# Optimization experiments

Measured on AMD Instinct MI355X. Metric: run time of the kernel, lower is better.

## Reference

```python
import jax, jax.numpy as jnp
import numpy as np

N_NODES = 65536
IN_DIM = 256
HIDDEN = 256
NUM_GRAPHS = 128   # B = batch.max()+1; fixed by construction in setup_inputs
MAX_LEN = 1024     # >= max per-graph length (avg 512, binomial tail << 1024)


def _uniform(key, shape, scale):
    return jax.random.uniform(key, shape, jnp.float32, -scale, scale)


def setup_inputs() -> dict:
    key = jax.random.key(0)
    ks = jax.random.split(key, 12)
    x = jax.random.normal(ks[0], (N_NODES, IN_DIM), jnp.float32)
    batch = jnp.sort(jax.random.randint(ks[1], (N_NODES,), 0, NUM_GRAPHS)).astype(jnp.int64)
    s = 1.0 / np.sqrt(HIDDEN)  # torch nn.GRU init: U(-1/sqrt(H), 1/sqrt(H))
    # gate order follows torch: (r, z, n) stacked along first axis -> 3H rows
    params = {
        'W_ih0': _uniform(ks[2], (3 * HIDDEN, IN_DIM), s),
        'W_hh0': _uniform(ks[3], (3 * HIDDEN, HIDDEN), s),
        'b_ih0': _uniform(ks[4], (3 * HIDDEN,), s),
        'b_hh0': _uniform(ks[5], (3 * HIDDEN,), s),
        'W_ih1': _uniform(ks[6], (3 * HIDDEN, HIDDEN), s),
        'W_hh1': _uniform(ks[7], (3 * HIDDEN, HIDDEN), s),
        'b_ih1': _uniform(ks[8], (3 * HIDDEN,), s),
        'b_hh1': _uniform(ks[9], (3 * HIDDEN,), s),
    }
    return {'x': x, 'batch': batch, **params}


def _gru_layer(xs, W_ih, W_hh, b_ih, b_hh):
    # xs: [B, L, D] -> [B, L, H]; torch GRU cell math, gate order (r, z, n)
    B = xs.shape[0]
    H = W_hh.shape[1]
    gx = jnp.einsum('bld,gd->blg', xs, W_ih) + b_ih  # precompute input gates, one big GEMM

    def step(h, gx_t):
        gh = h @ W_hh.T + b_hh
        xr, xz, xn = jnp.split(gx_t, 3, axis=-1)
        hr, hz, hn = jnp.split(gh, 3, axis=-1)
        r = jax.nn.sigmoid(xr + hr)
        z = jax.nn.sigmoid(xz + hz)
        n = jnp.tanh(xn + r * hn)
        h_new = (1.0 - z) * n + z * h
        return h_new, h_new

    h0 = jnp.zeros((B, H), xs.dtype)
    _, hs = jax.lax.scan(step, h0, jnp.swapaxes(gx, 0, 1))  # [L, B, H]
    return jnp.swapaxes(hs, 0, 1)


def reference(x, batch, W_ih0, W_hh0, b_ih0, b_hh0, W_ih1, W_hh1, b_ih1, b_hh1):
    # Ragged per-graph sequences -> padded [B, MAX_LEN, D]. Padding is at the
    # end of each row; GRU is causal so valid positions match the per-graph
    # loop in the original module exactly, and the masked mean ignores padding.
    N, D = x.shape
    b32 = batch.astype(jnp.int32)
    counts = jax.ops.segment_sum(jnp.ones((N,), jnp.float32), b32, num_segments=NUM_GRAPHS)
    starts = jnp.cumsum(counts) - counts              # exclusive prefix sum
    pos = jnp.arange(N, dtype=jnp.float32) - starts[b32]
    pos = pos.astype(jnp.int32)                       # position within graph

    xp = jnp.zeros((NUM_GRAPHS, MAX_LEN, D), x.dtype).at[b32, pos].set(x)
    mask = jnp.zeros((NUM_GRAPHS, MAX_LEN), x.dtype).at[b32, pos].set(1.0)

    h = _gru_layer(xp, W_ih0, W_hh0, b_ih0, b_hh0)
    h = _gru_layer(h, W_ih1, W_hh1, b_ih1, b_hh1)

    denom = jnp.maximum(counts, 1.0)[:, None]
    out = jnp.sum(h * mask[:, :, None], axis=1) / denom  # mean over valid steps
    return out  # dropout is identity at eval
```

## Files before the change

### kernel.cpp

```cpp
#include <hip/hip_runtime.h>
#include <hip/hip_bf16.h>

typedef _Float16 half2_t __attribute__((ext_vector_type(2)));
typedef _Float16 f16x8   __attribute__((ext_vector_type(8)));
typedef float    f32x4   __attribute__((ext_vector_type(4)));
typedef unsigned short u16;
typedef unsigned int   u32;

#define N_NODES 65536
#define IN_DIM  256
#define HIDDEN  256
#define G3      768
#define NGRAPH  128

__device__ __forceinline__ float sigf(float x)    { return 1.f / (1.f + __expf(-x)); }
__device__ __forceinline__ float tanhfast(float x){ return 2.f / (1.f + __expf(-2.f * x)) - 1.f; }

__device__ __forceinline__ void mfma_a(f32x4& acc, const f16x8& a, const f16x8& b) {
    asm("v_mfma_f32_16x16x32_f16 %0, %1, %2, %0" : "+v"(acc) : "a"(a), "v"(b));
}
__device__ __forceinline__ void mfma_v(f32x4& acc, const f16x8& a, const f16x8& b) {
    asm("v_mfma_f32_16x16x32_f16 %0, %1, %2, %0" : "+v"(acc) : "v"(a), "v"(b));
}
__device__ __forceinline__ void mfma_az(f32x4& acc, const f16x8& a, const f16x8& b, const f32x4& z) {
    asm("v_mfma_f32_16x16x32_f16 %0, %1, %2, %3" : "=&v"(acc) : "a"(a), "v"(b), "v"(z));
}
__device__ __forceinline__ void mfma_vz(f32x4& acc, const f16x8& a, const f16x8& b, const f32x4& z) {
    asm("v_mfma_f32_16x16x32_f16 %0, %1, %2, %3" : "=&v"(acc) : "v"(a), "v"(b), "v"(z));
}

__device__ __forceinline__ void wg_barrier_lds() {
    asm volatile("s_waitcnt lgkmcnt(0)" ::: "memory");
    __builtin_amdgcn_s_barrier();
}

__global__ void k_starts(const int* __restrict__ batch, int* __restrict__ starts, int n, int ngraph) {
    int g = blockIdx.x * blockDim.x + threadIdx.x;
    if (g > ngraph) return;
    int stride = (batch[n - 1] == 0) ? 2 : 1;
    if (g == ngraph) { starts[g] = n; return; }
    int lo = 0, hi = n;
    while (lo < hi) { int mid = (lo + hi) >> 1; if (batch[(size_t)mid * stride] < g) lo = mid + 1; else hi = mid; }
    starts[g] = lo;
}

__global__ void k_cvt8(const float* __restrict__ s, u16* __restrict__ d, int n) {
    int t = blockIdx.x * 256 + threadIdx.x;
    int i = t * 8;
    if (i >= n) return;
    float4 a = ((const float4*)(s + i))[0];
    float4 b = ((const float4*)(s + i))[1];
    f16x8 o;
    o[0] = (_Float16)a.x; o[1] = (_Float16)a.y; o[2] = (_Float16)a.z; o[3] = (_Float16)a.w;
    o[4] = (_Float16)b.x; o[5] = (_Float16)b.y; o[6] = (_Float16)b.z; o[7] = (_Float16)b.w;
    *(f16x8*)(d + i) = o;
}

__global__ void k_bias(const float* __restrict__ bih, const float* __restrict__ bhh, float* __restrict__ o) {
    int i = blockIdx.x * 256 + threadIdx.x;
    if (i < G3) o[i] = bih[i] + (i < 512 ? bhh[i] : 0.f);
}

__global__ void k_swz(const float* __restrict__ W, uint4* __restrict__ out) {
    int t = blockIdx.x * 256 + threadIdx.x;
    if (t >= 24576) return;
    int l = t & 63, c = t >> 6;
    int kt = c & 7, t6 = (c >> 3) % 12, wv = c / 96;
    int rg = t6 >> 2, sub = t6 & 3;
    int row = rg * 256 + wv * 64 + sub * 16 + (l & 15);
    int col = kt * 32 + (l >> 4) * 8;
    const float* s = W + row * 256 + col;
    f16x8 o;
#pragma unroll
    for (int q = 0; q < 8; q++) o[q] = (_Float16)s[q];
    out[t] = __builtin_bit_cast(uint4, o);
}

template <typename AT>
__global__ __launch_bounds__(256) void k_gemm(
    const AT* __restrict__ A, const u16* __restrict__ Bm,
    const float* __restrict__ bias, u16* __restrict__ C,
    int M, int N, int K)
{
    __shared__ u16 As[128 * 40];
    __shared__ u16 Bs[128 * 40];
    const int m0 = blockIdx.y * 128, n0 = blockIdx.x * 128;
    const int t = threadIdx.x;
    const int wave = t >> 6, lane = t & 63;
    const int wm = wave & 1, wn = wave >> 1;
    const int lr = lane & 15, lq = lane >> 4;
    f32x4 acc[4][4] = {};
    const int sr = t >> 1, sp = t & 1;
    const AT*  gA = A  + (size_t)(m0 + sr) * K + sp * 16;
    const u16* gB = Bm + (size_t)(n0 + sr) * K + sp * 16;
    u16* sA = As + sr * 40 + sp * 16;
    u16* sB = Bs + sr * 40 + sp * 16;
    for (int kt = 0; kt < K; kt += 32) {
        uint4 av0, av1;
        if constexpr (sizeof(AT) == 4) {
            float4 a0 = ((const float4*)gA)[0], a1 = ((const float4*)gA)[1];
            float4 a2 = ((const float4*)gA)[2], a3 = ((const float4*)gA)[3];
            f16x8 lo, hi;
            lo[0]=(_Float16)a0.x; lo[1]=(_Float16)a0.y; lo[2]=(_Float16)a0.z; lo[3]=(_Float16)a0.w;
            lo[4]=(_Float16)a1.x; lo[5]=(_Float16)a1.y; lo[6]=(_Float16)a1.z; lo[7]=(_Float16)a1.w;
            hi[0]=(_Float16)a2.x; hi[1]=(_Float16)a2.y; hi[2]=(_Float16)a2.z; hi[3]=(_Float16)a2.w;
            hi[4]=(_Float16)a3.x; hi[5]=(_Float16)a3.y; hi[6]=(_Float16)a3.z; hi[7]=(_Float16)a3.w;
            av0 = __builtin_bit_cast(uint4, lo);
            av1 = __builtin_bit_cast(uint4, hi);
        } else {
            av0 = ((const uint4*)gA)[0];
            av1 = ((const uint4*)gA)[1];
        }
        uint4 b0 = ((const uint4*)gB)[0], b1 = ((const uint4*)gB)[1];
        gA += 32; gB += 32;
        __syncthreads();
        ((uint4*)sA)[0] = av0; ((uint4*)sA)[1] = av1;
        ((uint4*)sB)[0] = b0;  ((uint4*)sB)[1] = b1;
        __syncthreads();
        f16x8 af[4], bf[4];
#pragma unroll
        for (int i = 0; i < 4; i++)
            af[i] = *(const f16x8*)(As + (wm * 64 + i * 16 + lr) * 40 + lq * 8);
#pragma unroll
        for (int j = 0; j < 4; j++)
            bf[j] = *(const f16x8*)(Bs + (wn * 64 + j * 16 + lr) * 40 + lq * 8);
#pragma unroll
        for (int i = 0; i < 4; i++)
#pragma unroll
            for (int j = 0; j < 4; j++)
                acc[i][j] = __builtin_amdgcn_mfma_f32_16x16x32_f16(af[i], bf[j], acc[i][j], 0, 0, 0);
    }
#pragma unroll
    for (int i = 0; i < 4; i++) {
        int row = m0 + wm * 64 + i * 16 + lq * 4;
#pragma unroll
        for (int j = 0; j < 4; j++) {
            int col = n0 + wn * 64 + j * 16 + lr;
            float bv = bias[col];
#pragma unroll
            for (int rr = 0; rr < 4; rr++) {
                _Float16 v = (_Float16)(acc[i][j][rr] + bv);
                C[(size_t)(row + rr) * N + col] = __builtin_bit_cast(u16, v);
            }
        }
    }
}

__global__ __attribute__((amdgpu_flat_work_group_size(256, 256), amdgpu_waves_per_eu(1, 1)))
void k_rec(
    const u16* __restrict__ gx,
    const uint4* __restrict__ wsw,
    const float* __restrict__ bhh,
    const int*   __restrict__ starts,
    u16* __restrict__ hout,
    float* __restrict__ out)
{
    __shared__ float gates[G3];
    __shared__ uint4 hbuf[2][HIDDEN / 8];
    const int g = blockIdx.x;
    const int tid = threadIdx.x;
    const int l = tid & 63, wv = tid >> 6;
    const int start = starts[g];
    const int len = starts[g + 1] - start;
    if (tid < HIDDEN / 8) hbuf[0][tid] = make_uint4(0, 0, 0, 0);
    f16x8 wa[60], wb[36];
    {
        const uint4* p = wsw + (size_t)wv * 96 * 64 + l;
#pragma unroll
        for (int f = 0; f < 60; f++) {
            f16x8 v = __builtin_bit_cast(f16x8, p[f * 64]);
            asm volatile("" : "+a"(v));
            wa[f] = v;
        }
#pragma unroll
        for (int f = 0; f < 36; f++) {
            f16x8 v = __builtin_bit_cast(f16x8, p[(60 + f) * 64]);
            asm volatile("" : "+v"(v));
            wb[f] = v;
        }
    }
    const _Float16* gxr = (const _Float16*)gx + (size_t)start * G3 + tid;
    u16* hb = hout ? (hout + (size_t)start * HIDDEN + tid) : (u16*)nullptr;
    float hp = 0.f, hs = 0.f;
    const float bn = bhh[512 + tid];
    const f32x4 zf = {0.f, 0.f, 0.f, 0.f};
    float c_r = 0.f, c_z = 0.f, c_n = 0.f;
    float n_r = 0.f, n_z = 0.f, n_n = 0.f;
    if (len > 0) {
        c_r = (float)gxr[0]; c_z = (float)gxr[256]; c_n = (float)gxr[512];
        int t1 = len > 1 ? 1 : 0;
        const _Float16* p = gxr + (u32)t1 * G3;
        n_r = (float)p[0]; n_z = (float)p[256]; n_n = (float)p[512];
    }
    __syncthreads();
    for (int t = 0; t < len; ++t) {
        int t2 = t + 2 < len ? t + 2 : len - 1;
        const _Float16* pp = gxr + (u32)t2 * G3;
        float l_r = (float)pp[0], l_z = (float)pp[256], l_n = (float)pp[512];
        f32x4 acc[12];
#pragma unroll
        for (int kt = 0; kt < 8; kt++) {
            f16x8 b = __builtin_bit_cast(f16x8, hbuf[t & 1][kt * 4 + (l >> 4)]);
#pragma unroll
            for (int t6 = 0; t6 < 12; t6++) {
                const int f = t6 * 8 + kt;
                if (kt == 0) {
                    if (f < 60) mfma_az(acc[t6], wa[f], b, zf);
                    else        mfma_vz(acc[t6], wb[f - 60], b, zf);
                } else {
                    if (f < 60) mfma_a(acc[t6], wa[f], b);
                    else        mfma_v(acc[t6], wb[f - 60], b);
                }
            }
        }
        asm volatile("s_nop 7\n\ts_nop 7"
                     : "+v"(acc[0]), "+v"(acc[1]), "+v"(acc[2]), "+v"(acc[3]),
                       "+v"(acc[4]), "+v"(acc[5]), "+v"(acc[6]), "+v"(acc[7]),
                       "+v"(acc[8]), "+v"(acc[9]), "+v"(acc[10]), "+v"(acc[11]));
        if ((l & 15) == 0) {
#pragma unroll
            for (int t6 = 0; t6 < 12; t6++) {
                int ro = (t6 >> 2) * 256 + wv * 64 + (t6 & 3) * 16 + (l >> 4) * 4;
                *(f32x4*)&gates[ro] = acc[t6];
            }
        }
        {
            float r = sigf(c_r + gates[tid]);
            float z = sigf(c_z + gates[256 + tid]);
            float n = tanhfast(c_n + r * (gates[512 + tid] + bn));
            float hnew = (1.f - z) * n + z * hp;
            hp = hnew; hs += hnew;
            _Float16 ph = (_Float16)hnew;
            u16 pk = __builtin_bit_cast(u16, ph);
            ((u16*)hbuf[(t + 1) & 1])[tid] = pk;
            if (hb) hb[(u32)t * HIDDEN] = pk;
            c_r = n_r; c_z = n_z; c_n = n_n;
            n_r = l_r; n_z = l_z; n_n = l_n;
        }
        wg_barrier_lds();
    }
    if (out) {
        float inv = 1.f / (float)(len > 0 ? len : 1);
        out[g * HIDDEN + tid] = hs * inv;
    }
}

extern "C" void kernel_launch(void* const* d_in, const int* in_sizes, int n_in,
                              void* d_out, int out_size, void* d_ws, size_t ws_size,
                              hipStream_t stream)
{
    const float* x     = (const float*)d_in[0];
    const int*   batch = (const int*)d_in[1];
    const float* Wih0  = (const float*)d_in[2];
    const float* Whh0  = (const float*)d_in[3];
    const float* bih0  = (const float*)d_in[4];
    const float* bhh0  = (const float*)d_in[5];
    const float* Wih1  = (const float*)d_in[6];
    const float* Whh1  = (const float*)d_in[7];
    const float* bih1  = (const float*)d_in[8];
    const float* bhh1  = (const float*)d_in[9];
    float* out = (float*)d_out;

    char* ws = (char*)d_ws;
    size_t o = 0;
    int*   starts = (int*)  (ws + o); o += 4096;
    float* bias0  = (float*)(ws + o); o += 4096;
    float* bias1  = (float*)(ws + o); o += 4096;
    u16*   wi0    = (u16*)  (ws + o); o += (size_t)G3 * IN_DIM * 2;
    u16*   wi1    = (u16*)  (ws + o); o += (size_t)G3 * HIDDEN * 2;
    uint4* wsw0   = (uint4*)(ws + o); o += (size_t)G3 * HIDDEN * 2;
    uint4* wsw1   = (uint4*)(ws + o); o += (size_t)G3 * HIDDEN * 2;
    u16*   h0     = (u16*)  (ws + o); o += (size_t)N_NODES * HIDDEN * 2;
    u16*   gxbuf  = (u16*)  (ws + o); o += (size_t)N_NODES * G3 * 2;

    k_starts<<<1, 256, 0, stream>>>(batch, starts, N_NODES, NGRAPH);
    k_bias<<<3, 256, 0, stream>>>(bih0, bhh0, bias0);
    k_bias<<<3, 256, 0, stream>>>(bih1, bhh1, bias1);
    k_cvt8<<<96, 256, 0, stream>>>(Wih0, wi0, G3 * IN_DIM);
    k_cvt8<<<96, 256, 0, stream>>>(Wih1, wi1, G3 * HIDDEN);
    k_swz<<<96, 256, 0, stream>>>(Whh0, wsw0);
    k_swz<<<96, 256, 0, stream>>>(Whh1, wsw1);

    k_gemm<float><<<dim3(G3 / 128, N_NODES / 128), 256, 0, stream>>>(x, wi0, bias0, gxbuf, N_NODES, G3, IN_DIM);
    k_rec<<<NGRAPH, 256, 0, stream>>>(gxbuf, wsw0, bhh0, starts, h0, (float*)nullptr);
    k_gemm<_Float16><<<dim3(G3 / 128, N_NODES / 128), 256, 0, stream>>>((const _Float16*)h0, wi1, bias1, gxbuf, N_NODES, G3, HIDDEN);
    k_rec<<<NGRAPH, 256, 0, stream>>>(gxbuf, wsw1, bhh1, starts, (u16*)nullptr, out);
}
```

Before: 1.782 ms.

## Interleave two graphs per recurrent block to overlap MFMA with gate math

Each recurrent workgroup now handles two graphs, A and B, and alternates between them. The MFMA matvec for one graph is issued while the elementwise gate update of the other runs, which hides MFMA latency and the barrier stall behind independent work. The grid is halved, so only 64 blocks run on the many CUs and each block's time is the longer of its two graphs' lengths. Sched barriers are added around the workgroup barrier, and the AGPR/VGPR weight split moves from 60/36 to 64/32.

Result: slower. 3.755 ms (+110.7%).

```diff
diff --git a/kernel.cpp b/kernel.cpp
--- a/kernel.cpp
+++ b/kernel.cpp
@@ -30,8 +30,11 @@
 }
 
 __device__ __forceinline__ void wg_barrier_lds() {
+    __builtin_amdgcn_sched_barrier(0);
     asm volatile("s_waitcnt lgkmcnt(0)" ::: "memory");
+    __builtin_amdgcn_sched_barrier(0);
     __builtin_amdgcn_s_barrier();
+    __builtin_amdgcn_sched_barrier(0);
 }
 
 __global__ void k_starts(const int* __restrict__ batch, int* __restrict__ starts, int n, int ngraph) {
@@ -155,93 +158,106 @@
     u16* __restrict__ hout,
     float* __restrict__ out)
 {
-    __shared__ float gates[G3];
-    __shared__ uint4 hbuf[2][HIDDEN / 8];
-    const int g = blockIdx.x;
+    __shared__ float gatesA[G3], gatesB[G3];
+    __shared__ uint4 hbA[2][HIDDEN / 8], hbB[2][HIDDEN / 8];
     const int tid = threadIdx.x;
     const int l = tid & 63, wv = tid >> 6;
-    const int start = starts[g];
-    const int len = starts[g + 1] - start;
-    if (tid < HIDDEN / 8) hbuf[0][tid] = make_uint4(0, 0, 0, 0);
-    f16x8 wa[60], wb[36];
+    const int gA = blockIdx.x, gB = blockIdx.x + NGRAPH / 2;
+    const int startA = starts[gA], lenA = starts[gA + 1] - startA;
+    const int startB = starts[gB], lenB = starts[gB + 1] - startB;
+    if (tid < HIDDEN / 8) { hbA[0][tid] = make_uint4(0,0,0,0); hbB[0][tid] = make_uint4(0,0,0,0); }
+    f16x8 wa[64], wb[32];
     {
         const uint4* p = wsw + (size_t)wv * 96 * 64 + l;
 #pragma unroll
-        for (int f = 0; f < 60; f++) {
+        for (int f = 0; f < 64; f++) {
             f16x8 v = __builtin_bit_cast(f16x8, p[f * 64]);
             asm volatile("" : "+a"(v));
             wa[f] = v;
         }
 #pragma unroll
-        for (int f = 0; f < 36; f++) {
-            f16x8 v = __builtin_bit_cast(f16x8, p[(60 + f) * 64]);
+        for (int f = 0; f < 32; f++) {
+            f16x8 v = __builtin_bit_cast(f16x8, p[(64 + f) * 64]);
             asm volatile("" : "+v"(v));
             wb[f] = v;
         }
     }
-    const _Float16* gxr = (const _Float16*)gx + (size_t)start * G3 + tid;
-    u16* hb = hout ? (hout + (size_t)start * HIDDEN + tid) : (u16*)nullptr;
-    float hp = 0.f, hs = 0.f;
+    const _Float16* gxrA = (const _Float16*)gx + (size_t)startA * G3 + tid;
+    const _Float16* gxrB = (const _Float16*)gx + (size_t)startB * G3 + tid;
+    u16* hoA = hout ? (hout + (size_t)startA * HIDDEN + tid) : (u16*)nullptr;
+    u16* hoB = hout ? (hout + (size_t)startB * HIDDEN + tid) : (u16*)nullptr;
     const float bn = bhh[512 + tid];
     const f32x4 zf = {0.f, 0.f, 0.f, 0.f};
-    float c_r = 0.f, c_z = 0.f, c_n = 0.f;
-    float n_r = 0.f, n_z = 0.f, n_n = 0.f;
-    if (len > 0) {
-        c_r = (float)gxr[0]; c_z = (float)gxr[256]; c_n = (float)gxr[512];
-        int t1 = len > 1 ? 1 : 0;
-        const _Float16* p = gxr + (u32)t1 * G3;
-        n_r = (float)p[0]; n_z = (float)p[256]; n_n = (float)p[512];
-    }
+    float hpA = 0.f, hsA = 0.f, hpB = 0.f, hsB = 0.f;
+    float aR = 0.f, aZ = 0.f, aN = 0.f, bR = 0.f, bZ = 0.f, bN = 0.f;
+    if (lenA > 0) { aR = (float)gxrA[0]; aZ = (float)gxrA[256]; aN = (float)gxrA[512]; }
+    if (lenB > 0) { bR = (float)gxrB[0]; bZ = (float)gxrB[256]; bN = (float)gxrB[512]; }
+    f32x4 accA[12], accB[12];
+
+#define MFMA_STEP(ACC, HBBUF)                                                   \
+    do {                                                                        \
+        _Pragma("unroll")                                                       \
+        for (int kt = 0; kt < 8; kt++) {                                        \
+            f16x8 b = __builtin_bit_cast(f16x8, (HBBUF)[kt * 4 + (l >> 4)]);    \
+            _Pragma("unroll")                                                   \
+            for (int t6 = 0; t6 < 12; t6++) {                                   \
+                const int f = t6 * 8 + kt;                                      \
+                if (kt == 0) { if (f < 64) mfma_az(ACC[t6], wa[f], b, zf);      \
+                               else        mfma_vz(ACC[t6], wb[f - 64], b, zf);}\
+                else         { if (f < 64) mfma_a(ACC[t6], wa[f], b);           \
+                               else        mfma_v(ACC[t6], wb[f - 64], b); }    \
+            }                                                                   \
+        }                                                                       \
+    } while (0)
+
+#define NOP_FENCE(ACC)                                                          \
+    asm volatile("s_nop 7\n\ts_nop 7"                                           \
+                 : "+v"(ACC[0]), "+v"(ACC[1]), "+v"(ACC[2]), "+v"(ACC[3]),      \
+                   "+v"(ACC[4]), "+v"(ACC[5]), "+v"(ACC[6]), "+v"(ACC[7]),      \
+                   "+v"(ACC[8]), "+v"(ACC[9]), "+v"(ACC[10]), "+v"(ACC[11]))
+
+#define FIN_STEP(ACC, GATES, HBARR, CR, CZ, CN, HP, HS, HOP, GXR, LEN, I)       \
+    do {                                                                        \
+        int inx_ = (I) + 1 < (LEN) ? (I) + 1 : (LEN) - 1;                       \
+        const _Float16* pp_ = (GXR) + (u32)inx_ * G3;                           \
+        float pR_ = (float)pp_[0], pZ_ = (float)pp_[256], pN_ = (float)pp_[512];\
+        NOP_FENCE(ACC);                                                         \
+        if ((l & 15) == 0) {                                                    \
+            _Pragma("unroll")                                                   \
+            for (int t6 = 0; t6 < 12; t6++) {                                   \
+                int ro = (t6 >> 2) * 256 + wv * 64 + (t6 & 3) * 16 + (l >> 4) * 4;\
+                *(f32x4*)&(GATES)[ro] = ACC[t6];                                \
+            }                                                                   \
+        }                                                                       \
+        float r_ = sigf((CR) + (GATES)[tid]);                                   \
+        float z_ = sigf((CZ) + (GATES)[256 + tid]);                             \
+        float n_ = tanhfast((CN) + r_ * ((GATES)[512 + tid] + bn));             \
+        float hn_ = (1.f - z_) * n_ + z_ * (HP);                                \
+        (HP) = hn_; (HS) += hn_;                                                \
+        _Float16 ph_ = (_Float16)hn_;                                           \
+        u16 pk_ = __builtin_bit_cast(u16, ph_);                                 \
+        ((u16*)(HBARR)[((I) + 1) & 1])[tid] = pk_;                              \
+        if (HOP) (HOP)[(u32)(I) * HIDDEN] = pk_;                                \
+        (CR) = pR_; (CZ) = pZ_; (CN) = pN_;                                     \
+    } while (0)
+
     __syncthreads();
-    for (int t = 0; t < len; ++t) {
-        int t2 = t + 2 < len ? t + 2 : len - 1;
-        const _Float16* pp = gxr + (u32)t2 * G3;
-        float l_r = (float)pp[0], l_z = (float)pp[256], l_n = (float)pp[512];
-        f32x4 acc[12];
-#pragma unroll
-        for (int kt = 0; kt < 8; kt++) {
-            f16x8 b = __builtin_bit_cast(f16x8, hbuf[t & 1][kt * 4 + (l >> 4)]);
-#pragma unroll
-            for (int t6 = 0; t6 < 12; t6++) {
-                const int f = t6 * 8 + kt;
-                if (kt == 0) {
-                    if (f < 60) mfma_az(acc[t6], wa[f], b, zf);
-                    else        mfma_vz(acc[t6], wb[f - 60], b, zf);
-                } else {
-                    if (f < 60) mfma_a(acc[t6], wa[f], b);
-                    else        mfma_v(acc[t6], wb[f - 60], b);
-                }
-            }
-        }
-        asm volatile("s_nop 7\n\ts_nop 7"
-                     : "+v"(acc[0]), "+v"(acc[1]), "+v"(acc[2]), "+v"(acc[3]),
-                       "+v"(acc[4]), "+v"(acc[5]), "+v"(acc[6]), "+v"(acc[7]),
-                       "+v"(acc[8]), "+v"(acc[9]), "+v"(acc[10]), "+v"(acc[11]));
-        if ((l & 15) == 0) {
-#pragma unroll
-            for (int t6 = 0; t6 < 12; t6++) {
-                int ro = (t6 >> 2) * 256 + wv * 64 + (t6 & 3) * 16 + (l >> 4) * 4;
-                *(f32x4*)&gates[ro] = acc[t6];
-            }
-        }
-        {
-            float r = sigf(c_r + gates[tid]);
-            float z = sigf(c_z + gates[256 + tid]);
-            float n = tanhfast(c_n + r * (gates[512 + tid] + bn));
-            float hnew = (1.f - z) * n + z * hp;
-            hp = hnew; hs += hnew;
-            _Float16 ph = (_Float16)hnew;
-            u16 pk = __builtin_bit_cast(u16, ph);
-            ((u16*)hbuf[(t + 1) & 1])[tid] = pk;
-            if (hb) hb[(u32)t * HIDDEN] = pk;
-            c_r = n_r; c_z = n_z; c_n = n_n;
-            n_r = l_r; n_z = l_z; n_n = l_n;
-        }
+    const int lenM = lenA > lenB ? lenA : lenB;
+    if (lenA > 0) MFMA_STEP(accA, hbA[0]);
+    for (int i = 0; i < lenM; ++i) {
+        if (i < lenB) MFMA_STEP(accB, hbB[i & 1]);
+        if (i < lenA) FIN_STEP(accA, gatesA, hbA, aR, aZ, aN, hpA, hsA, hoA, gxrA, lenA, i);
         wg_barrier_lds();
-    }
+        if (i + 1 < lenA) MFMA_STEP(accA, hbA[(i + 1) & 1]);
+        if (i < lenB) FIN_STEP(accB, gatesB, hbB, bR, bZ, bN, hpB, hsB, hoB, gxrB, lenB, i);
+        wg_barrier_lds();
+    }
+#undef MFMA_STEP
+#undef NOP_FENCE
+#undef FIN_STEP
     if (out) {
-        float inv = 1.f / (float)(len > 0 ? len : 1);
-        out[g * HIDDEN + tid] = hs * inv;
+        out[gA * HIDDEN + tid] = hsA / (float)(lenA > 0 ? lenA : 1);
+        out[gB * HIDDEN + tid] = hsB / (float)(lenB > 0 ? lenB : 1);
     }
 }
 
@@ -282,7 +298,7 @@
     k_swz<<<96, 256, 0, stream>>>(Whh1, wsw1);
 
     k_gemm<float><<<dim3(G3 / 128, N_NODES / 128), 256, 0, stream>>>(x, wi0, bias0, gxbuf, N_NODES, G3, IN_DIM);
-    k_rec<<<NGRAPH, 256, 0, stream>>>(gxbuf, wsw0, bhh0, starts, h0, (float*)nullptr);
+    k_rec<<<NGRAPH / 2, 256, 0, stream>>>(gxbuf, wsw0, bhh0, starts, h0, (float*)nullptr);
     k_gemm<_Float16><<<dim3(G3 / 128, N_NODES / 128), 256, 0, stream>>>((const _Float16*)h0, wi1, bias1, gxbuf, N_NODES, G3, HIDDEN);
-    k_rec<<<NGRAPH, 256, 0, stream>>>(gxbuf, wsw1, bhh1, starts, (u16*)nullptr, out);
-}
+    k_rec<<<NGRAPH / 2, 256, 0, stream>>>(gxbuf, wsw1, bhh1, starts, (u16*)nullptr, out);
+}
```
